# Kernel tuning notes

Measured on AMD Instinct MI355X. Metric: run time of the kernel, lower is better.

## Reference

```python
import jax, jax.numpy as jnp
import numpy as np

HDIM = 128
SCALE = HDIM ** (-0.5)


def setup_inputs() -> dict:
    key = jax.random.key(0)
    ks = jax.random.split(key, 6)
    B, H, I, J, D = 4, 16, 2048, 2048, HDIM
    q = jax.random.normal(ks[0], (B, H, I, D), dtype=jnp.float32)
    kv = jax.random.normal(ks[1], (B, H, J, D), dtype=jnp.float32)
    # torch nn.Linear weights stored as [out_features, in_features]
    Wq = jax.random.normal(ks[2], (D, D), dtype=jnp.float32) * (D ** -0.5)
    Wkv = jax.random.normal(ks[3], (2 * D, D), dtype=jnp.float32) * (D ** -0.5)
    Wout = jax.random.normal(ks[4], (D, D), dtype=jnp.float32) * (D ** -0.5)
    bout = jax.random.normal(ks[5], (D,), dtype=jnp.float32) * 0.01
    return {"q": q, "kv": kv, "Wq": Wq, "Wkv": Wkv, "Wout": Wout, "bout": bout}


def reference(q, kv, Wq, Wkv, Wout, bout):
    # projections (torch Linear: x @ W.T)
    qp = jnp.einsum('bhid,ed->bhie', q, Wq)
    kvp = jnp.einsum('bhjd,ed->bhje', kv, Wkv)
    k, v = jnp.split(kvp, 2, axis=-1)
    # scaled dot-product cross attention, full score matrix [b,h,i,j]
    dots = jnp.einsum('bhid,bhjd->bhij', qp, k) * SCALE
    attn = jax.nn.softmax(dots, axis=-1)
    out = jnp.einsum('bhij,bhjd->bhid', attn, v)
    # output projection (dropout is identity at inference)
    return jnp.einsum('bhid,ed->bhie', out, Wout) + bout
```

## Files before the change

kernel.cpp:

```cpp
#include <hip/hip_runtime.h>
#include <hip/hip_bf16.h>
#include <math.h>

typedef __attribute__((ext_vector_type(8))) short bf16x8;
typedef __attribute__((ext_vector_type(4))) unsigned short u16x4;
typedef __attribute__((ext_vector_type(4))) float f32x4;

#define MFMA16(a, b, c) __builtin_amdgcn_mfma_f32_16x16x32_bf16(a, b, c, 0, 0, 0)

__device__ inline unsigned short f2bf(float x) {
  union { float f; unsigned u; } v; v.f = x;
  unsigned r = v.u + 0x7FFFu + ((v.u >> 16) & 1u);
  return (unsigned short)(r >> 16);
}

__device__ inline float exp2a(float x) {
  float r;
  asm("v_exp_f32 %0, %1" : "=v"(r) : "v"(x));
  return r;
}

__device__ inline void dma16(const unsigned short* g, unsigned short* l) {
  __builtin_amdgcn_global_load_lds(
      (const __attribute__((address_space(1))) unsigned int*)g,
      (__attribute__((address_space(3))) unsigned int*)l, 16, 0, 0);
}

__device__ unsigned short g_wbf[65536];

__global__ __launch_bounds__(256) void conv_w(
    const float* __restrict__ Wq, const float* __restrict__ Wkv,
    const float* __restrict__ Wout)
{
  int idx = (blockIdx.x * 256 + threadIdx.x) * 4;
  const float* src; int off;
  if (idx < 16384)      { src = Wq;   off = idx; }
  else if (idx < 49152) { src = Wkv;  off = idx - 16384; }
  else                  { src = Wout; off = idx - 49152; }
  float4 v = *(const float4*)(src + off);
  u16x4 pk;
  pk.x = f2bf(v.x); pk.y = f2bf(v.y); pk.z = f2bf(v.z); pk.w = f2bf(v.w);
  *(u16x4*)&g_wbf[idx] = pk;
}

__global__ __launch_bounds__(256) void proj_q(
    const float* __restrict__ A, unsigned short* __restrict__ out0, float scale)
{
  const int mbase = blockIdx.x * 64;
  const unsigned short* Wb = g_wbf;

  __shared__ unsigned short a_s[64 * 136];
  __shared__ unsigned short w_s[128 * 136];

  const int tid = threadIdx.x;
  for (int p = 0; p < 8; ++p) {
    int r = p * 8 + (tid >> 5);
    int c = tid & 31;
    float4 v = ((const float4*)(A + (size_t)(mbase + r) * 128))[c];
    u16x4 pk;
    pk.x = f2bf(v.x); pk.y = f2bf(v.y); pk.z = f2bf(v.z); pk.w = f2bf(v.w);
    *(u16x4*)&a_s[r * 136 + c * 4] = pk;
  }
  {
    int r0 = tid >> 4, c = (tid & 15) * 8;
    for (int p = 0; p < 8; ++p) {
      int r = p * 16 + r0;
      *(bf16x8*)&w_s[r * 136 + c] = *(const bf16x8*)(Wb + (size_t)r * 128 + c);
    }
  }
  __syncthreads();

  const int wave = tid >> 6, lane = tid & 63, quad = lane >> 4, lr = lane & 15;
  f32x4 zero = {0.f, 0.f, 0.f, 0.f};
  f32x4 acc[8];
  for (int nb = 0; nb < 8; ++nb) acc[nb] = zero;
  for (int ks = 0; ks < 4; ++ks) {
    bf16x8 af = *(const bf16x8*)&a_s[(wave * 16 + lr) * 136 + ks * 32 + quad * 8];
    for (int nb = 0; nb < 8; ++nb) {
      bf16x8 bf = *(const bf16x8*)&w_s[(nb * 16 + lr) * 136 + ks * 32 + quad * 8];
      acc[nb] = MFMA16(af, bf, acc[nb]);
    }
  }
  for (int nb = 0; nb < 8; ++nb)
    for (int r = 0; r < 4; ++r) {
      int row = mbase + wave * 16 + quad * 4 + r;
      int col = nb * 16 + lr;
      out0[(size_t)row * 128 + col] = f2bf(acc[nb][r] * scale);
    }
}

__global__ __launch_bounds__(256) void proj_kv(
    const float* __restrict__ A,
    unsigned short* __restrict__ outK, unsigned short* __restrict__ outVT)
{
  const int mbase = blockIdx.x * 64;
  __shared__ unsigned short a_s[64 * 136];
  __shared__ unsigned short w_s[128 * 136];
  const int tid = threadIdx.x;

  for (int p = 0; p < 8; ++p) {
    int r = p * 8 + (tid >> 5);
    int c = tid & 31;
    float4 v = ((const float4*)(A + (size_t)(mbase + r) * 128))[c];
    u16x4 pk;
    pk.x = f2bf(v.x); pk.y = f2bf(v.y); pk.z = f2bf(v.z); pk.w = f2bf(v.w);
    *(u16x4*)&a_s[r * 136 + c * 4] = pk;
  }

  const int wave = tid >> 6, lane = tid & 63, quad = lane >> 4, lr = lane & 15;
  f32x4 zero = {0.f, 0.f, 0.f, 0.f};

  for (int nt = 0; nt < 2; ++nt) {
    __syncthreads();
    {
      const unsigned short* Wb = g_wbf + 16384 + nt * 16384;
      int r0 = tid >> 4, c = (tid & 15) * 8;
      for (int p = 0; p < 8; ++p) {
        int r = p * 16 + r0;
        *(bf16x8*)&w_s[r * 136 + c] = *(const bf16x8*)(Wb + (size_t)r * 128 + c);
      }
    }
    __syncthreads();

    f32x4 acc[8];
    for (int nb = 0; nb < 8; ++nb) acc[nb] = zero;
    for (int ks = 0; ks < 4; ++ks) {
      bf16x8 af = *(const bf16x8*)&a_s[(wave * 16 + lr) * 136 + ks * 32 + quad * 8];
      for (int nb = 0; nb < 8; ++nb) {
        bf16x8 bf = *(const bf16x8*)&w_s[(nb * 16 + lr) * 136 + ks * 32 + quad * 8];
        acc[nb] = MFMA16(af, bf, acc[nb]);
      }
    }

    if (nt == 0) {
      for (int nb = 0; nb < 8; ++nb)
        for (int r = 0; r < 4; ++r) {
          int row = mbase + wave * 16 + quad * 4 + r;
          int col = nb * 16 + lr;
          outK[(size_t)row * 128 + col] = f2bf(acc[nb][r]);
        }
    } else {
      int gm = mbase + wave * 16 + quad * 4;
      int bh = gm >> 11;
      int j  = gm & 2047;
      unsigned short* vt = outVT + (size_t)bh * 128 * 2048;
      for (int nb = 0; nb < 8; ++nb) {
        int col = nb * 16 + lr;
        u16x4 pk;
        pk.x = f2bf(acc[nb][0]); pk.y = f2bf(acc[nb][1]);
        pk.z = f2bf(acc[nb][2]); pk.w = f2bf(acc[nb][3]);
        *(u16x4*)&vt[(size_t)col * 2048 + j] = pk;
      }
    }
  }
}

__global__ __launch_bounds__(512, 2) void attn_fused(
    const unsigned short* __restrict__ qp,
    const unsigned short* __restrict__ kb,
    const unsigned short* __restrict__ vTb,
    unsigned short* __restrict__ ao)
{
  const int xcd = blockIdx.x & 7;
  const int loc = blockIdx.x >> 3;
  const int qt  = loc & 7;
  const int bh  = (loc >> 3) * 8 + xcd;
  const unsigned short* Q  = qp  + (size_t)bh * 2048 * 128 + (size_t)qt * 256 * 128;
  const unsigned short* K  = kb  + (size_t)bh * 2048 * 128;
  const unsigned short* VT = vTb + (size_t)bh * 128 * 2048;
  unsigned short* AO = ao + (size_t)bh * 2048 * 128 + (size_t)qt * 256 * 128;

  __shared__ unsigned short k_s [2][64 * 128];
  __shared__ unsigned short vT_s[2][128 * 64];
  __shared__ unsigned short p_s [256 * 64];
  __shared__ float redu_s[8][2][16];

  const int tid = threadIdx.x;
  const int wave = tid >> 6, lane = tid & 63, quad = lane >> 4, lr = lane & 15;

  const int kw_i = wave * 2;
  const int rk0  = 4 * kw_i + (lane >> 4);
  const int rk1  = 4 * (kw_i + 1) + (lane >> 4);
  const int kgo0 = rk0 * 128 + ((lane & 15) ^ (rk0 & 15)) * 8;
  const int kgo1 = rk1 * 128 + ((lane & 15) ^ (rk1 & 15)) * 8;
  const int rv0  = 8 * kw_i + (lane >> 3);
  const int rv1  = 8 * (kw_i + 1) + (lane >> 3);
  const int vsc  = ((lane & 7) ^ ((lane >> 3) & 7)) * 8;
  const int vgo0 = rv0 * 2048 + vsc;
  const int vgo1 = rv1 * 2048 + vsc;
  const int klds0 = kw_i * 512, klds1 = kw_i * 512 + 512;

#define ISSUE_K(T, BUF) do { \
    const unsigned short* _kt = K + (size_t)(T) * 8192; \
    dma16(_kt + kgo0, &k_s[BUF][klds0]); \
    dma16(_kt + kgo1, &k_s[BUF][klds1]); } while (0)
#define ISSUE_V(T, BUF) do { \
    const unsigned short* _vt = VT + (size_t)(T) * 64; \
    dma16(_vt + vgo0, &vT_s[BUF][klds0]); \
    dma16(_vt + vgo1, &vT_s[BUF][klds1]); } while (0)

  bf16x8 qf[2][4];
#pragma unroll
  for (int mb = 0; mb < 2; ++mb)
#pragma unroll
    for (int ks = 0; ks < 4; ++ks)
      qf[mb][ks] = *(const bf16x8*)(Q + (size_t)(wave * 32 + mb * 16 + lr) * 128 + ks * 32 + quad * 8);
  __builtin_amdgcn_sched_barrier(0);
  ISSUE_K(0, 0);
  ISSUE_V(0, 0);
  ISSUE_K(1, 1);
  __builtin_amdgcn_sched_barrier(0);

  f32x4 zero = {0.f, 0.f, 0.f, 0.f};
  f32x4 o_acc[2][8];
  float m_i[2], l_i[2];
#pragma unroll
  for (int mb = 0; mb < 2; ++mb) {
#pragma unroll
    for (int db = 0; db < 8; ++db) o_acc[mb][db] = zero;
    m_i[mb] = -1e30f; l_i[mb] = 0.f;
  }
  int rescM = 0;

  asm volatile("s_waitcnt vmcnt(2)" ::: "memory");
  __builtin_amdgcn_s_barrier();
  __builtin_amdgcn_sched_barrier(0);
  ISSUE_V(1, 1);

#define STEP(JT, BUF) do { \
    f32x4 sT[2][4]; \
    _Pragma("unroll") \
    for (int mi = 0; mi < 2; ++mi) \
      _Pragma("unroll") \
      for (int jb = 0; jb < 4; ++jb) sT[mi][jb] = zero; \
    __builtin_amdgcn_s_setprio(1); \
    _Pragma("unroll") \
    for (int ks = 0; ks < 4; ++ks) { \
      _Pragma("unroll") \
      for (int jb = 0; jb < 4; ++jb) { \
        bf16x8 kfj = *(const bf16x8*)&k_s[BUF][(jb * 16 + lr) * 128 + (((ks * 4 + quad) ^ lr) << 3)]; \
        sT[0][jb] = MFMA16(kfj, qf[0][ks], sT[0][jb]); \
        sT[1][jb] = MFMA16(kfj, qf[1][ks], sT[1][jb]); \
      } \
    } \
    __builtin_amdgcn_s_setprio(0); \
    _Pragma("unroll") \
    for (int mi = 0; mi < 2; ++mi) { \
      const int mb = mi; \
      float mx = fmaxf(fmaxf(sT[mi][0][0], sT[mi][0][1]), fmaxf(sT[mi][0][2], sT[mi][0][3])); \
      _Pragma("unroll") \
      for (int jb = 1; jb < 4; ++jb) \
        mx = fmaxf(mx, fmaxf(fmaxf(sT[mi][jb][0], sT[mi][jb][1]), \
                             fmaxf(sT[mi][jb][2], sT[mi][jb][3]))); \
      mx = fmaxf(mx, __shfl_xor(mx, 16)); \
      mx = fmaxf(mx, __shfl_xor(mx, 32)); \
      if (!__all(mx - m_i[mb] <= 8.f)) {            \
        float mnew = fmaxf(m_i[mb], mx); \
        float alpha = exp2a(m_i[mb] - mnew); \
        m_i[mb] = mnew; \
        l_i[mb] *= alpha; \
        if (lane < 16) redu_s[wave][mb][lane] = alpha; \
        rescM |= (1 << (mb)); \
      } \
      float rs = 0.f; \
      const int prow = wave * 32 + mb * 16 + lr; \
      _Pragma("unroll") \
      for (int jb = 0; jb < 4; ++jb) { \
        float p0 = exp2a(sT[mi][jb][0] - m_i[mb]); \
        float p1 = exp2a(sT[mi][jb][1] - m_i[mb]); \
        float p2 = exp2a(sT[mi][jb][2] - m_i[mb]); \
        float p3 = exp2a(sT[mi][jb][3] - m_i[mb]); \
        rs += (p0 + p1) + (p2 + p3); \
        u16x4 pk; \
        pk.x = f2bf(p0); pk.y = f2bf(p1); pk.z = f2bf(p2); pk.w = f2bf(p3); \
        int c = jb * 2 + (quad >> 1); \
        *(u16x4*)&p_s[prow * 64 + ((c ^ (lr & 7)) << 3) + ((quad & 1) << 2)] = pk; \
      } \
      rs += __shfl_xor(rs, 16); \
      rs += __shfl_xor(rs, 32); \
      l_i[mb] += rs; \
    } \
    __builtin_amdgcn_s_barrier();         \
    __builtin_amdgcn_sched_barrier(0); \
    if ((JT) <= 29) ISSUE_K((JT) + 2, BUF); \
    _Pragma("unroll") \
    for (int mb = 0; mb < 2; ++mb) \
      if (rescM & (1 << (mb))) {                       \
        f32x4 av = *(const f32x4*)&redu_s[wave][mb][quad * 4]; \
        _Pragma("unroll") \
        for (int db = 0; db < 8; ++db) o_acc[mb][db] *= av; \
      } \
    rescM = 0; \
    __builtin_amdgcn_s_setprio(1); \
    _Pragma("unroll") \
    for (int ks2 = 0; ks2 < 2; ++ks2) { \
      const int pc = ((ks2 * 4 + quad) ^ (lr & 7)) << 3; \
      bf16x8 pf[2]; \
      _Pragma("unroll") \
      for (int mb = 0; mb < 2; ++mb) \
        pf[mb] = *(const bf16x8*)&p_s[(wave * 32 + mb * 16 + lr) * 64 + pc]; \
      _Pragma("unroll") \
      for (int db = 0; db < 8; ++db) { \
        bf16x8 vf = *(const bf16x8*)&vT_s[BUF][(db * 16 + lr) * 64 + pc]; \
        _Pragma("unroll") \
        for (int mb = 0; mb < 2; ++mb) \
          o_acc[mb][db] = MFMA16(pf[mb], vf, o_acc[mb][db]); \
      } \
    } \
    __builtin_amdgcn_s_setprio(0); \
    if ((JT) >= 30) { asm volatile("s_waitcnt vmcnt(0)" ::: "memory"); } \
    else            { asm volatile("s_waitcnt vmcnt(2)" ::: "memory"); } \
    __builtin_amdgcn_s_barrier();         \
    __builtin_amdgcn_sched_barrier(0); \
    if ((JT) <= 29) ISSUE_V((JT) + 2, BUF); \
  } while (0)

#pragma unroll 1
  for (int jtb = 0; jtb < 16; ++jtb) {
    const int jt0 = jtb * 2;
    STEP(jt0, 0);
    STEP(jt0 + 1, 1);
  }
#undef STEP
#undef ISSUE_K
#undef ISSUE_V

#pragma unroll
  for (int mb = 0; mb < 2; ++mb)
    if (lane < 16) redu_s[wave][mb][lane] = l_i[mb];
#pragma unroll
  for (int mb = 0; mb < 2; ++mb) {
    f32x4 l4 = *(const f32x4*)&redu_s[wave][mb][quad * 4];
#pragma unroll
    for (int r = 0; r < 4; ++r) {
      float inv = 1.f / l4[r];
      int row = wave * 32 + mb * 16 + quad * 4 + r;
#pragma unroll
      for (int db = 0; db < 8; ++db)
        AO[(size_t)row * 128 + db * 16 + lr] = f2bf(o_acc[mb][db][r] * inv);
    }
  }
}

__global__ __launch_bounds__(256) void proj_out_k(
    const unsigned short* __restrict__ A,
    const float* __restrict__ bias, float* __restrict__ out)
{
  const int mbase = blockIdx.x * 64;
  const unsigned short* Wb = g_wbf + 49152;
  __shared__ unsigned short a_s[64 * 136];
  __shared__ unsigned short w_s[128 * 136];
  const int tid = threadIdx.x;
  {
    int r0 = tid >> 4, c = (tid & 15) * 8;
    for (int p = 0; p < 4; ++p)
      *(bf16x8*)&a_s[(p * 16 + r0) * 136 + c] =
          *(const bf16x8*)(A + (size_t)(mbase + p * 16 + r0) * 128 + c);
    for (int p = 0; p < 8; ++p)
      *(bf16x8*)&w_s[(p * 16 + r0) * 136 + c] =
          *(const bf16x8*)(Wb + (size_t)(p * 16 + r0) * 128 + c);
  }
  __syncthreads();
  const int wave = tid >> 6, lane = tid & 63, quad = lane >> 4, lr = lane & 15;
  f32x4 zero = {0.f, 0.f, 0.f, 0.f};
  f32x4 acc[8];
  for (int nb = 0; nb < 8; ++nb) acc[nb] = zero;
  for (int ks = 0; ks < 4; ++ks) {
    bf16x8 af = *(const bf16x8*)&a_s[(wave * 16 + lr) * 136 + ks * 32 + quad * 8];
    for (int nb = 0; nb < 8; ++nb) {
      bf16x8 bf = *(const bf16x8*)&w_s[(nb * 16 + lr) * 136 + ks * 32 + quad * 8];
      acc[nb] = MFMA16(af, bf, acc[nb]);
    }
  }
  for (int nb = 0; nb < 8; ++nb)
    for (int r = 0; r < 4; ++r) {
      int row = mbase + wave * 16 + quad * 4 + r;
      int col = nb * 16 + lr;
      out[(size_t)row * 128 + col] = acc[nb][r] + bias[col];
    }
}

extern "C" void kernel_launch(void* const* d_in, const int* in_sizes, int n_in,
                              void* d_out, int out_size, void* d_ws, size_t ws_size,
                              hipStream_t stream) {
  const float* q    = (const float*)d_in[0];
  const float* kv   = (const float*)d_in[1];
  const float* Wq   = (const float*)d_in[2];
  const float* Wkv  = (const float*)d_in[3];
  const float* Wout = (const float*)d_in[4];
  const float* bout = (const float*)d_in[5];
  float* out = (float*)d_out;

  const size_t NELEM = (size_t)131072 * 128;
  unsigned short* qp_b = (unsigned short*)d_ws;
  unsigned short* k_b  = qp_b + NELEM;
  unsigned short* vT_b = k_b + NELEM;
  unsigned short* ao_b = vT_b + NELEM;

  const float SCALE2 = 0.08838834764831845f * 1.4426950408889634f;

  conv_w<<<dim3(64), 256, 0, stream>>>(Wq, Wkv, Wout);
  proj_q<<<dim3(2048), 256, 0, stream>>>(q, qp_b, SCALE2);
  proj_kv<<<dim3(2048), 256, 0, stream>>>(kv, k_b, vT_b);
  attn_fused<<<dim3(512), 512, 0, stream>>>(qp_b, k_b, vT_b, ao_b);
  proj_out_k<<<dim3(2048), 256, 0, stream>>>(ao_b, bout, out);
}
```

Measured before the change: 382.8 us.

## Fuse Q and KV projections into one launch and stage V transpose through LDS

Removes the separate weight-conversion kernel and merges the Q and KV projection kernels into a single 4096-block launch, with each block converting fp32 weights to bf16 on the fly. This cuts launch count and lets the Q and KV work fill the GPU together. The V-transpose store now goes through shared memory so each thread writes contiguous 16-byte chunks to global memory instead of scattered 8-byte stores. In exchange, every block re-reads and re-converts fp32 weights, which adds redundant global traffic and conversion work.

Measured after the change: 389.8 us. No clear change (+1.8%).

```diff
diff --git a/kernel.cpp b/kernel.cpp
--- a/kernel.cpp
+++ b/kernel.cpp
@@ -26,99 +26,36 @@
       (__attribute__((address_space(3))) unsigned int*)l, 16, 0, 0);
 }
 
-__device__ unsigned short g_wbf[65536];
-
-__global__ __launch_bounds__(256) void conv_w(
+__global__ __launch_bounds__(256) void proj_qkv(
+    const float* __restrict__ Aq, const float* __restrict__ Akv,
     const float* __restrict__ Wq, const float* __restrict__ Wkv,
-    const float* __restrict__ Wout)
+    unsigned short* __restrict__ outQ, unsigned short* __restrict__ outK,
+    unsigned short* __restrict__ outVT, float scale)
 {
-  int idx = (blockIdx.x * 256 + threadIdx.x) * 4;
-  const float* src; int off;
-  if (idx < 16384)      { src = Wq;   off = idx; }
-  else if (idx < 49152) { src = Wkv;  off = idx - 16384; }
-  else                  { src = Wout; off = idx - 49152; }
-  float4 v = *(const float4*)(src + off);
-  u16x4 pk;
-  pk.x = f2bf(v.x); pk.y = f2bf(v.y); pk.z = f2bf(v.z); pk.w = f2bf(v.w);
-  *(u16x4*)&g_wbf[idx] = pk;
-}
-
-__global__ __launch_bounds__(256) void proj_q(
-    const float* __restrict__ A, unsigned short* __restrict__ out0, float scale)
-{
-  const int mbase = blockIdx.x * 64;
-  const unsigned short* Wb = g_wbf;
-
   __shared__ unsigned short a_s[64 * 136];
   __shared__ unsigned short w_s[128 * 136];
 
   const int tid = threadIdx.x;
-  for (int p = 0; p < 8; ++p) {
-    int r = p * 8 + (tid >> 5);
-    int c = tid & 31;
-    float4 v = ((const float4*)(A + (size_t)(mbase + r) * 128))[c];
-    u16x4 pk;
-    pk.x = f2bf(v.x); pk.y = f2bf(v.y); pk.z = f2bf(v.z); pk.w = f2bf(v.w);
-    *(u16x4*)&a_s[r * 136 + c * 4] = pk;
-  }
-  {
-    int r0 = tid >> 4, c = (tid & 15) * 8;
-    for (int p = 0; p < 8; ++p) {
-      int r = p * 16 + r0;
-      *(bf16x8*)&w_s[r * 136 + c] = *(const bf16x8*)(Wb + (size_t)r * 128 + c);
-    }
-  }
-  __syncthreads();
-
   const int wave = tid >> 6, lane = tid & 63, quad = lane >> 4, lr = lane & 15;
   f32x4 zero = {0.f, 0.f, 0.f, 0.f};
-  f32x4 acc[8];
-  for (int nb = 0; nb < 8; ++nb) acc[nb] = zero;
-  for (int ks = 0; ks < 4; ++ks) {
-    bf16x8 af = *(const bf16x8*)&a_s[(wave * 16 + lr) * 136 + ks * 32 + quad * 8];
-    for (int nb = 0; nb < 8; ++nb) {
-      bf16x8 bf = *(const bf16x8*)&w_s[(nb * 16 + lr) * 136 + ks * 32 + quad * 8];
-      acc[nb] = MFMA16(af, bf, acc[nb]);
-    }
-  }
-  for (int nb = 0; nb < 8; ++nb)
-    for (int r = 0; r < 4; ++r) {
-      int row = mbase + wave * 16 + quad * 4 + r;
-      int col = nb * 16 + lr;
-      out0[(size_t)row * 128 + col] = f2bf(acc[nb][r] * scale);
-    }
-}
-
-__global__ __launch_bounds__(256) void proj_kv(
-    const float* __restrict__ A,
-    unsigned short* __restrict__ outK, unsigned short* __restrict__ outVT)
-{
-  const int mbase = blockIdx.x * 64;
-  __shared__ unsigned short a_s[64 * 136];
-  __shared__ unsigned short w_s[128 * 136];
-  const int tid = threadIdx.x;
-
-  for (int p = 0; p < 8; ++p) {
-    int r = p * 8 + (tid >> 5);
-    int c = tid & 31;
-    float4 v = ((const float4*)(A + (size_t)(mbase + r) * 128))[c];
-    u16x4 pk;
-    pk.x = f2bf(v.x); pk.y = f2bf(v.y); pk.z = f2bf(v.z); pk.w = f2bf(v.w);
-    *(u16x4*)&a_s[r * 136 + c * 4] = pk;
-  }
-
-  const int wave = tid >> 6, lane = tid & 63, quad = lane >> 4, lr = lane & 15;
-  f32x4 zero = {0.f, 0.f, 0.f, 0.f};
-
-  for (int nt = 0; nt < 2; ++nt) {
-    __syncthreads();
-    {
-      const unsigned short* Wb = g_wbf + 16384 + nt * 16384;
-      int r0 = tid >> 4, c = (tid & 15) * 8;
-      for (int p = 0; p < 8; ++p) {
-        int r = p * 16 + r0;
-        *(bf16x8*)&w_s[r * 136 + c] = *(const bf16x8*)(Wb + (size_t)r * 128 + c);
-      }
+
+  if (blockIdx.x < 2048) {
+    const int mbase = blockIdx.x * 64;
+    for (int p = 0; p < 8; ++p) {
+      int r = p * 8 + (tid >> 5);
+      int c = tid & 31;
+      float4 v = ((const float4*)(Aq + (size_t)(mbase + r) * 128))[c];
+      u16x4 pk;
+      pk.x = f2bf(v.x); pk.y = f2bf(v.y); pk.z = f2bf(v.z); pk.w = f2bf(v.w);
+      *(u16x4*)&a_s[r * 136 + c * 4] = pk;
+    }
+    for (int p = 0; p < 16; ++p) {
+      int r = p * 8 + (tid >> 5);
+      int c = tid & 31;
+      float4 v = ((const float4*)(Wq + (size_t)r * 128))[c];
+      u16x4 pk;
+      pk.x = f2bf(v.x); pk.y = f2bf(v.y); pk.z = f2bf(v.z); pk.w = f2bf(v.w);
+      *(u16x4*)&w_s[r * 136 + c * 4] = pk;
     }
     __syncthreads();
 
@@ -131,25 +68,72 @@
         acc[nb] = MFMA16(af, bf, acc[nb]);
       }
     }
-
-    if (nt == 0) {
-      for (int nb = 0; nb < 8; ++nb)
-        for (int r = 0; r < 4; ++r) {
-          int row = mbase + wave * 16 + quad * 4 + r;
-          int col = nb * 16 + lr;
-          outK[(size_t)row * 128 + col] = f2bf(acc[nb][r]);
+    for (int nb = 0; nb < 8; ++nb)
+      for (int r = 0; r < 4; ++r) {
+        int row = mbase + wave * 16 + quad * 4 + r;
+        int col = nb * 16 + lr;
+        outQ[(size_t)row * 128 + col] = f2bf(acc[nb][r] * scale);
+      }
+  } else {
+    const int mbase = (blockIdx.x - 2048) * 64;
+    for (int p = 0; p < 8; ++p) {
+      int r = p * 8 + (tid >> 5);
+      int c = tid & 31;
+      float4 v = ((const float4*)(Akv + (size_t)(mbase + r) * 128))[c];
+      u16x4 pk;
+      pk.x = f2bf(v.x); pk.y = f2bf(v.y); pk.z = f2bf(v.z); pk.w = f2bf(v.w);
+      *(u16x4*)&a_s[r * 136 + c * 4] = pk;
+    }
+
+    for (int nt = 0; nt < 2; ++nt) {
+      __syncthreads();
+      {
+        const float* Wb = Wkv + nt * 16384;
+        for (int p = 0; p < 16; ++p) {
+          int r = p * 8 + (tid >> 5);
+          int c = tid & 31;
+          float4 v = ((const float4*)(Wb + (size_t)r * 128))[c];
+          u16x4 pk;
+          pk.x = f2bf(v.x); pk.y = f2bf(v.y); pk.z = f2bf(v.z); pk.w = f2bf(v.w);
+          *(u16x4*)&w_s[r * 136 + c * 4] = pk;
         }
-    } else {
-      int gm = mbase + wave * 16 + quad * 4;
-      int bh = gm >> 11;
-      int j  = gm & 2047;
-      unsigned short* vt = outVT + (size_t)bh * 128 * 2048;
-      for (int nb = 0; nb < 8; ++nb) {
-        int col = nb * 16 + lr;
-        u16x4 pk;
-        pk.x = f2bf(acc[nb][0]); pk.y = f2bf(acc[nb][1]);
-        pk.z = f2bf(acc[nb][2]); pk.w = f2bf(acc[nb][3]);
-        *(u16x4*)&vt[(size_t)col * 2048 + j] = pk;
+      }
+      __syncthreads();
+
+      f32x4 acc[8];
+      for (int nb = 0; nb < 8; ++nb) acc[nb] = zero;
+      for (int ks = 0; ks < 4; ++ks) {
+        bf16x8 af = *(const bf16x8*)&a_s[(wave * 16 + lr) * 136 + ks * 32 + quad * 8];
+        for (int nb = 0; nb < 8; ++nb) {
+          bf16x8 bf = *(const bf16x8*)&w_s[(nb * 16 + lr) * 136 + ks * 32 + quad * 8];
+          acc[nb] = MFMA16(af, bf, acc[nb]);
+        }
+      }
+
+      if (nt == 0) {
+        for (int nb = 0; nb < 8; ++nb)
+          for (int r = 0; r < 4; ++r) {
+            int row = mbase + wave * 16 + quad * 4 + r;
+            int col = nb * 16 + lr;
+            outK[(size_t)row * 128 + col] = f2bf(acc[nb][r]);
+          }
+      } else {
+        unsigned short* t_s = w_s;
+        __syncthreads();
+        const int jloc = wave * 16 + quad * 4;
+        for (int nb = 0; nb < 8; ++nb) {
+          u16x4 pk;
+          pk.x = f2bf(acc[nb][0]); pk.y = f2bf(acc[nb][1]);
+          pk.z = f2bf(acc[nb][2]); pk.w = f2bf(acc[nb][3]);
+          *(u16x4*)&t_s[(nb * 16 + lr) * 72 + jloc] = pk;
+        }
+        __syncthreads();
+        const int col = tid >> 1, hf = (tid & 1) * 32;
+        unsigned short* vt = outVT + (size_t)(mbase >> 11) * 128 * 2048
+                             + (size_t)col * 2048 + (mbase & 2047) + hf;
+        const unsigned short* ts = &t_s[col * 72 + hf];
+        for (int k2 = 0; k2 < 4; ++k2)
+          *(bf16x8*)(vt + k2 * 8) = *(const bf16x8*)(ts + k2 * 8);
       }
     }
   }
@@ -343,11 +327,10 @@
 }
 
 __global__ __launch_bounds__(256) void proj_out_k(
-    const unsigned short* __restrict__ A,
+    const unsigned short* __restrict__ A, const float* __restrict__ Wout,
     const float* __restrict__ bias, float* __restrict__ out)
 {
   const int mbase = blockIdx.x * 64;
-  const unsigned short* Wb = g_wbf + 49152;
   __shared__ unsigned short a_s[64 * 136];
   __shared__ unsigned short w_s[128 * 136];
   const int tid = threadIdx.x;
@@ -356,9 +339,14 @@
     for (int p = 0; p < 4; ++p)
       *(bf16x8*)&a_s[(p * 16 + r0) * 136 + c] =
           *(const bf16x8*)(A + (size_t)(mbase + p * 16 + r0) * 128 + c);
-    for (int p = 0; p < 8; ++p)
-      *(bf16x8*)&w_s[(p * 16 + r0) * 136 + c] =
-          *(const bf16x8*)(Wb + (size_t)(p * 16 + r0) * 128 + c);
+  }
+  for (int p = 0; p < 16; ++p) {
+    int r = p * 8 + (tid >> 5);
+    int c = tid & 31;
+    float4 v = ((const float4*)(Wout + (size_t)r * 128))[c];
+    u16x4 pk;
+    pk.x = f2bf(v.x); pk.y = f2bf(v.y); pk.z = f2bf(v.z); pk.w = f2bf(v.w);
+    *(u16x4*)&w_s[r * 136 + c * 4] = pk;
   }
   __syncthreads();
   const int wave = tid >> 6, lane = tid & 63, quad = lane >> 4, lr = lane & 15;
@@ -399,9 +387,7 @@
 
   const float SCALE2 = 0.08838834764831845f * 1.4426950408889634f;
 
-  conv_w<<<dim3(64), 256, 0, stream>>>(Wq, Wkv, Wout);
-  proj_q<<<dim3(2048), 256, 0, stream>>>(q, qp_b, SCALE2);
-  proj_kv<<<dim3(2048), 256, 0, stream>>>(kv, k_b, vT_b);
+  proj_qkv<<<dim3(4096), 256, 0, stream>>>(q, kv, Wq, Wkv, qp_b, k_b, vT_b, SCALE2);
   attn_fused<<<dim3(512), 512, 0, stream>>>(qp_b, k_b, vT_b, ao_b);
-  proj_out_k<<<dim3(2048), 256, 0, stream>>>(ao_b, bout, out);
-}
+  proj_out_k<<<dim3(2048), 256, 0, stream>>>(ao_b, Wout, bout, out);
+}
```

## Fuse output projection and bias into attention kernel epilogue

Applied to the files above, without the earlier changes.

The attention kernel now converts Wout to bf16 in shared memory after the main loop. It normalizes the output accumulators, stages them as bf16 through the existing P buffer, and runs the output-projection MFMAs directly, writing fp32 results with bias. This removes the separate proj_out kernel and the round trip of the attention output through global memory. In exchange it adds about 34 KB of LDS per block, which may reduce occupancy, and adds epilogue work to the long-running attention kernel.

After: 372.9 us. -2.6%, faster.

```diff
diff --git a/kernel.cpp b/kernel.cpp
--- a/kernel.cpp
+++ b/kernel.cpp
@@ -26,17 +26,15 @@
       (__attribute__((address_space(3))) unsigned int*)l, 16, 0, 0);
 }
 
-__device__ unsigned short g_wbf[65536];
+__device__ unsigned short g_wbf[49152];
 
 __global__ __launch_bounds__(256) void conv_w(
-    const float* __restrict__ Wq, const float* __restrict__ Wkv,
-    const float* __restrict__ Wout)
+    const float* __restrict__ Wq, const float* __restrict__ Wkv)
 {
   int idx = (blockIdx.x * 256 + threadIdx.x) * 4;
   const float* src; int off;
-  if (idx < 16384)      { src = Wq;   off = idx; }
-  else if (idx < 49152) { src = Wkv;  off = idx - 16384; }
-  else                  { src = Wout; off = idx - 49152; }
+  if (idx < 16384) { src = Wq;  off = idx; }
+  else             { src = Wkv; off = idx - 16384; }
   float4 v = *(const float4*)(src + off);
   u16x4 pk;
   pk.x = f2bf(v.x); pk.y = f2bf(v.y); pk.z = f2bf(v.z); pk.w = f2bf(v.w);
@@ -159,7 +157,9 @@
     const unsigned short* __restrict__ qp,
     const unsigned short* __restrict__ kb,
     const unsigned short* __restrict__ vTb,
-    unsigned short* __restrict__ ao)
+    const float* __restrict__ Wout,
+    const float* __restrict__ bias,
+    float* __restrict__ out)
 {
   const int xcd = blockIdx.x & 7;
   const int loc = blockIdx.x >> 3;
@@ -168,12 +168,13 @@
   const unsigned short* Q  = qp  + (size_t)bh * 2048 * 128 + (size_t)qt * 256 * 128;
   const unsigned short* K  = kb  + (size_t)bh * 2048 * 128;
   const unsigned short* VT = vTb + (size_t)bh * 128 * 2048;
-  unsigned short* AO = ao + (size_t)bh * 2048 * 128 + (size_t)qt * 256 * 128;
+  float* OUT = out + (size_t)bh * 2048 * 128 + (size_t)qt * 256 * 128;
 
   __shared__ unsigned short k_s [2][64 * 128];
   __shared__ unsigned short vT_s[2][128 * 64];
   __shared__ unsigned short p_s [256 * 64];
   __shared__ float redu_s[8][2][16];
+  __shared__ unsigned short wout_s[128 * 136];
 
   const int tid = threadIdx.x;
   const int wave = tid >> 6, lane = tid & 63, quad = lane >> 4, lr = lane & 15;
@@ -326,57 +327,82 @@
 #undef ISSUE_V
 
 #pragma unroll
+  for (int p = 0; p < 4; ++p) {
+    int r = p * 32 + (tid >> 4);
+    int c = (tid & 15) * 8;
+    float4 v0 = *(const float4*)(Wout + (size_t)r * 128 + c);
+    float4 v1 = *(const float4*)(Wout + (size_t)r * 128 + c + 4);
+    u16x4 pk0, pk1;
+    pk0.x = f2bf(v0.x); pk0.y = f2bf(v0.y); pk0.z = f2bf(v0.z); pk0.w = f2bf(v0.w);
+    pk1.x = f2bf(v1.x); pk1.y = f2bf(v1.y); pk1.z = f2bf(v1.z); pk1.w = f2bf(v1.w);
+    *(u16x4*)&wout_s[r * 136 + c] = pk0;
+    *(u16x4*)&wout_s[r * 136 + c + 4] = pk1;
+  }
+
+#pragma unroll
   for (int mb = 0; mb < 2; ++mb)
     if (lane < 16) redu_s[wave][mb][lane] = l_i[mb];
 #pragma unroll
   for (int mb = 0; mb < 2; ++mb) {
     f32x4 l4 = *(const f32x4*)&redu_s[wave][mb][quad * 4];
-#pragma unroll
-    for (int r = 0; r < 4; ++r) {
-      float inv = 1.f / l4[r];
-      int row = wave * 32 + mb * 16 + quad * 4 + r;
-#pragma unroll
-      for (int db = 0; db < 8; ++db)
-        AO[(size_t)row * 128 + db * 16 + lr] = f2bf(o_acc[mb][db][r] * inv);
-    }
-  }
-}
-
-__global__ __launch_bounds__(256) void proj_out_k(
-    const unsigned short* __restrict__ A,
-    const float* __restrict__ bias, float* __restrict__ out)
-{
-  const int mbase = blockIdx.x * 64;
-  const unsigned short* Wb = g_wbf + 49152;
-  __shared__ unsigned short a_s[64 * 136];
-  __shared__ unsigned short w_s[128 * 136];
-  const int tid = threadIdx.x;
-  {
-    int r0 = tid >> 4, c = (tid & 15) * 8;
-    for (int p = 0; p < 4; ++p)
-      *(bf16x8*)&a_s[(p * 16 + r0) * 136 + c] =
-          *(const bf16x8*)(A + (size_t)(mbase + p * 16 + r0) * 128 + c);
-    for (int p = 0; p < 8; ++p)
-      *(bf16x8*)&w_s[(p * 16 + r0) * 136 + c] =
-          *(const bf16x8*)(Wb + (size_t)(p * 16 + r0) * 128 + c);
-  }
+    f32x4 invv;
+#pragma unroll
+    for (int r = 0; r < 4; ++r) invv[r] = 1.f / l4[r];
+#pragma unroll
+    for (int db = 0; db < 8; ++db) o_acc[mb][db] *= invv;
+  }
+
   __syncthreads();
-  const int wave = tid >> 6, lane = tid & 63, quad = lane >> 4, lr = lane & 15;
-  f32x4 zero = {0.f, 0.f, 0.f, 0.f};
-  f32x4 acc[8];
-  for (int nb = 0; nb < 8; ++nb) acc[nb] = zero;
-  for (int ks = 0; ks < 4; ++ks) {
-    bf16x8 af = *(const bf16x8*)&a_s[(wave * 16 + lr) * 136 + ks * 32 + quad * 8];
+
+  f32x4 acc2[2][8];
+#pragma unroll
+  for (int mb = 0; mb < 2; ++mb)
+#pragma unroll
+    for (int nb = 0; nb < 8; ++nb) acc2[mb][nb] = zero;
+
+#pragma unroll
+  for (int h = 0; h < 2; ++h) {
+#pragma unroll
+    for (int mb = 0; mb < 2; ++mb)
+#pragma unroll
+      for (int db2 = 0; db2 < 4; ++db2) {
+        f32x4 o = o_acc[mb][h * 4 + db2];
+#pragma unroll
+        for (int r = 0; r < 4; ++r) {
+          int row = mb * 16 + quad * 4 + r;
+          int colh = db2 * 16 + lr;
+          int chunk = colh >> 3, off = colh & 7;
+          p_s[(wave * 32 + row) * 64 + ((chunk ^ (row & 7)) << 3) + off] = f2bf(o[r]);
+        }
+      }
+#pragma unroll
+    for (int ks = 0; ks < 2; ++ks) {
+#pragma unroll
+      for (int mb = 0; mb < 2; ++mb) {
+        int arow = mb * 16 + lr;
+        int kk = ks * 32 + quad * 8;
+        int chunk = kk >> 3;
+        bf16x8 af = *(const bf16x8*)&p_s[(wave * 32 + arow) * 64 + ((chunk ^ (arow & 7)) << 3)];
+#pragma unroll
+        for (int nb = 0; nb < 8; ++nb) {
+          bf16x8 bf = *(const bf16x8*)&wout_s[(nb * 16 + lr) * 136 + h * 64 + kk];
+          acc2[mb][nb] = MFMA16(af, bf, acc2[mb][nb]);
+        }
+      }
+    }
+  }
+
+#pragma unroll
+  for (int mb = 0; mb < 2; ++mb)
+#pragma unroll
     for (int nb = 0; nb < 8; ++nb) {
-      bf16x8 bf = *(const bf16x8*)&w_s[(nb * 16 + lr) * 136 + ks * 32 + quad * 8];
-      acc[nb] = MFMA16(af, bf, acc[nb]);
-    }
-  }
-  for (int nb = 0; nb < 8; ++nb)
-    for (int r = 0; r < 4; ++r) {
-      int row = mbase + wave * 16 + quad * 4 + r;
       int col = nb * 16 + lr;
-      out[(size_t)row * 128 + col] = acc[nb][r] + bias[col];
+      float b = bias[col];
+#pragma unroll
+      for (int r = 0; r < 4; ++r) {
+        int row = wave * 32 + mb * 16 + quad * 4 + r;
+        OUT[(size_t)row * 128 + col] = acc2[mb][nb][r] + b;
+      }
     }
 }
 
@@ -395,13 +421,11 @@
   unsigned short* qp_b = (unsigned short*)d_ws;
   unsigned short* k_b  = qp_b + NELEM;
   unsigned short* vT_b = k_b + NELEM;
-  unsigned short* ao_b = vT_b + NELEM;
 
   const float SCALE2 = 0.08838834764831845f * 1.4426950408889634f;
 
-  conv_w<<<dim3(64), 256, 0, stream>>>(Wq, Wkv, Wout);
+  conv_w<<<dim3(48), 256, 0, stream>>>(Wq, Wkv);
   proj_q<<<dim3(2048), 256, 0, stream>>>(q, qp_b, SCALE2);
   proj_kv<<<dim3(2048), 256, 0, stream>>>(kv, k_b, vT_b);
-  attn_fused<<<dim3(512), 512, 0, stream>>>(qp_b, k_b, vT_b, ao_b);
-  proj_out_k<<<dim3(2048), 256, 0, stream>>>(ao_b, bout, out);
-}
+  attn_fused<<<dim3(512), 512, 0, stream>>>(qp_b, k_b, vT_b, Wout, bout, out);
+}
```
